# Kernel optimization log

Hardware: AMD Instinct MI355X
Metric: run time of the kernel (lower is better)

## Reference

```python
import jax, jax.numpy as jnp
import numpy as np

B, N, M, D = 4096, 39, 32, 32   # batch, fields, embed_dim, product_layer_dim
F = 1_000_000                   # features_dim (sparse vocab)
H = [400, 400, 400]             # hidden layer sizes
BN_EPS = 1e-3                   # keras BatchNormalization default epsilon


def setup_inputs() -> dict:
    key = jax.random.key(0)
    ks = jax.random.split(key, 32)
    inp = {
        "feature_index": jax.random.randint(ks[0], (B, N), 0, F),
        "feature_value": jax.random.normal(ks[1], (B, N), dtype=jnp.float32),
        # keras Embedding default 'uniform' initializer: U(-0.05, 0.05)
        "emb_table": jax.random.uniform(ks[2], (F, M), minval=-0.05, maxval=0.05, dtype=jnp.float32),
        "lin_w": jax.random.normal(ks[3], (D, N, M), dtype=jnp.float32) * 0.05,
        "quad_w": jax.random.normal(ks[4], (D, N), dtype=jnp.float32) * 0.1,
    }
    # MLP: input is concat(l_z, l_p) -> 2*D wide
    dims = [2 * D] + H
    k = 5
    for i in range(len(H)):
        fan_in, fan_out = dims[i], dims[i + 1]
        scale = (2.0 / (fan_in + fan_out)) ** 0.5
        inp[f"W{i}"] = jax.random.normal(ks[k], (fan_in, fan_out), dtype=jnp.float32) * scale; k += 1
        inp[f"b{i}"] = jnp.zeros((fan_out,), jnp.float32)
        inp[f"g{i}"] = jnp.ones((fan_out,), jnp.float32)    # BN gamma
        inp[f"be{i}"] = jnp.zeros((fan_out,), jnp.float32)  # BN beta
        inp[f"rm{i}"] = jnp.zeros((fan_out,), jnp.float32)  # BN moving mean
        inp[f"rv{i}"] = jnp.ones((fan_out,), jnp.float32)   # BN moving var
    inp["Wout"] = jax.random.normal(ks[k], (H[-1], 1), dtype=jnp.float32) * 0.05
    inp["bout"] = jnp.zeros((1,), jnp.float32)
    return inp


def _forward(feature_index, emb_table, lin_w, quad_w, layer_params, Wout, bout):
    e = emb_table[feature_index]                          # (B, N, M) embedding lookup
    l_z = jnp.einsum('bnm,dnm->bd', e, lin_w)             # linear signal
    theta = jnp.einsum('bnm,dn->bdnm', e, quad_w)         # IPNN quadratic signal
    l_p = jnp.einsum('bdnm,bdnm->bd', theta, theta)       # sum of squares over (n, m)
    x = jnp.concatenate([l_z, l_p], axis=1)               # (B, 2D)
    for (W, b, g, be, rm, rv) in layer_params:
        x = x @ W + b
        x = (x - rm) * jax.lax.rsqrt(rv + BN_EPS) * g + be  # BN (inference stats)
        x = jax.nn.relu(x)
    return jax.nn.sigmoid(x @ Wout + bout)                # (B, 1)


def reference(feature_index, feature_value, emb_table, lin_w, quad_w,
              W0, b0, g0, be0, rm0, rv0,
              W1, b1, g1, be1, rm1, rv1,
              W2, b2, g2, be2, rm2, rv2,
              Wout, bout):
    # feature_value is accepted by the original call() but never used; dropout disabled (eval).
    layer_params = [
        (W0, b0, g0, be0, rm0, rv0),
        (W1, b1, g1, be1, rm1, rv1),
        (W2, b2, g2, be2, rm2, rv2),
    ]
    return _forward(feature_index, emb_table, lin_w, quad_w, layer_params, Wout, bout)
```

## Files before the change

kernel.cpp:

```cpp
#include <hip/hip_runtime.h>
#include <hip/hip_bf16.h>
#include <math.h>

#define TB 4096
#define TN 39
#define TM 32
#define TD 32
#define TH 400
#define BN_EPS 1e-3f

#define KT0 2
#define KTH 13

typedef __attribute__((ext_vector_type(8))) short bf16x8;
typedef __attribute__((ext_vector_type(4))) float f32x4;

__device__ __forceinline__ ushort bf16_rn(float x) {
    __hip_bfloat16 h = __float2bfloat16(x);
    union { __hip_bfloat16 b; ushort u; } c; c.b = h; return c.u;
}
__device__ __forceinline__ void split2(float x, ushort& hi, ushort& lo) {
    unsigned xb = __float_as_uint(x);
    unsigned hb = xb & 0xFFFF0000u;
    hi = (ushort)(hb >> 16);
    lo = bf16_rn(x - __uint_as_float(hb));
}

__device__ __forceinline__ size_t panel_idx(int p, int k, int KT) {
    int lane_ = (p & 15) + 16 * ((k >> 2) & 3);
    int j_    = (k & 3) + 4 * ((k >> 4) & 1);
    return (((size_t)((p >> 4) * KT + (k >> 5)) * 64) + lane_) * 8 + j_;
}

__global__ __launch_bounds__(256) void fused_front_kernel(
    const int*   __restrict__ fidx,
    const float* __restrict__ emb,
    const float* __restrict__ lin_w,
    const float* __restrict__ quad_w,
    const float* __restrict__ W0, const float* __restrict__ W1, const float* __restrict__ W2,
    const float* __restrict__ b0_, const float* __restrict__ g0_, const float* __restrict__ be0_,
    const float* __restrict__ rm0_, const float* __restrict__ rv0_,
    const float* __restrict__ b1_, const float* __restrict__ g1_, const float* __restrict__ be1_,
    const float* __restrict__ rm1_, const float* __restrict__ rv1_,
    const float* __restrict__ b2_, const float* __restrict__ g2_, const float* __restrict__ be2_,
    const float* __restrict__ rm2_, const float* __restrict__ rv2_,
    ushort* __restrict__ A0h, ushort* __restrict__ A0l,
    ushort* __restrict__ B0h, ushort* __restrict__ B0l,
    ushort* __restrict__ B1h, ushort* __restrict__ B1l,
    ushort* __restrict__ B2h, ushort* __restrict__ B2l,
    float* __restrict__ AC)
{
    if (blockIdx.x >= TB / 4) {
        int tid = (blockIdx.x - TB / 4) * 256 + threadIdx.x;
        const int NW0 = 64 * 112, NW = 416 * 112;
        if (tid < NW0 + 2 * NW) {
            const float* W; ushort *Ph, *Pl; int k, n4, K, KT;
            if (tid < NW0) {
                W = W0; Ph = B0h; Pl = B0l; k = tid / 112; n4 = tid % 112; K = 64; KT = KT0;
            } else if (tid < NW0 + NW) {
                int u = tid - NW0;
                W = W1; Ph = B1h; Pl = B1l; k = u / 112; n4 = u % 112; K = TH; KT = KTH;
            } else {
                int u = tid - NW0 - NW;
                W = W2; Ph = B2h; Pl = B2l; k = u / 112; n4 = u % 112; K = TH; KT = KTH;
            }
            int n0 = n4 * 4;
            float4 w = make_float4(0.f, 0.f, 0.f, 0.f);
            if (k < K && n0 < TH)
                w = *(const float4*)&W[(size_t)k * TH + n0];
            float vals[4] = {w.x, w.y, w.z, w.w};
            #pragma unroll
            for (int i = 0; i < 4; ++i) {
                ushort hi, lo; split2(vals[i], hi, lo);
                size_t idx = panel_idx(n0 + i, k, KT);
                Ph[idx] = hi; Pl[idx] = lo;
            }
        } else if (tid < NW0 + 2 * NW + 3 * 448) {
            int u = tid - NW0 - 2 * NW;
            int layer = u / 448, h = u % 448;
            const float *gp, *bep, *rmp, *rvp, *bp;
            if (layer == 0)      { gp = g0_; bep = be0_; rmp = rm0_; rvp = rv0_; bp = b0_; }
            else if (layer == 1) { gp = g1_; bep = be1_; rmp = rm1_; rvp = rv1_; bp = b1_; }
            else                 { gp = g2_; bep = be2_; rmp = rm2_; rvp = rv2_; bp = b2_; }
            float aj = 0.f, cj = 0.f;
            if (h < TH) {
                aj = gp[h] * rsqrtf(rvp[h] + BN_EPS);
                cj = (bp[h] - rmp[h]) * aj + bep[h];
            }
            AC[layer * 896 + h] = aj;
            AC[layer * 896 + 448 + h] = cj;
        }
        return;
    }

    constexpr int R = 4;
    __shared__ float e_s[R][TN * TM];
    __shared__ int   idx_s[R][TN];
    __shared__ float s_s[R][TN];

    const int t  = threadIdx.x;
    const int b0 = blockIdx.x * R;

    if (t < R * TN) {
        int r = t / TN, n = t - r * TN;
        idx_s[r][n] = fidx[(b0 + r) * TN + n];
    }
    __syncthreads();

    for (int r = 0; r < R; ++r) {
        for (int k4 = t; k4 < TN * TM / 4; k4 += 256) {
            int n = k4 >> 3;
            long long base = (long long)idx_s[r][n] * TM + ((k4 & 7) << 2);
            *(float4*)&e_s[r][k4 * 4] = *(const float4*)&emb[base];
        }
    }
    __syncthreads();

    {
        const int d = t >> 3, j = t & 7;
        float acc[R] = {0.f, 0.f, 0.f, 0.f};
        const float* lw_base = lin_w + d * (TN * TM);
        #pragma unroll 4
        for (int i = 0; i < TN; ++i) {
            float4 lw = *(const float4*)&lw_base[i * 32 + j * 4];
            #pragma unroll
            for (int r = 0; r < R; ++r) {
                float4 e4 = *(const float4*)&e_s[r][i * 32 + j * 4];
                acc[r] = fmaf(lw.x, e4.x, acc[r]);
                acc[r] = fmaf(lw.y, e4.y, acc[r]);
                acc[r] = fmaf(lw.z, e4.z, acc[r]);
                acc[r] = fmaf(lw.w, e4.w, acc[r]);
            }
        }
        #pragma unroll
        for (int off = 1; off < 8; off <<= 1)
            #pragma unroll
            for (int r = 0; r < R; ++r)
                acc[r] += __shfl_xor(acc[r], off);
        if (j == 0) {
            #pragma unroll
            for (int r = 0; r < R; ++r) {
                ushort hi, lo; split2(acc[r], hi, lo);
                size_t idx = panel_idx(b0 + r, d, KT0);
                A0h[idx] = hi; A0l[idx] = lo;
            }
        }
    }

    {
        int r = t >> 6, lane = t & 63;
        if (lane < TN) {
            float s = 0.f;
            #pragma unroll
            for (int mm = 0; mm < TM; ++mm) {
                float v = e_s[r][lane * TM + ((lane + mm) & 31)];
                s = fmaf(v, v, s);
            }
            s_s[r][lane] = s;
        }
    }
    __syncthreads();

    if (t < R * TD) {
        int r = t >> 5, d = t & 31;
        float accv = 0.f;
        for (int n = 0; n < TN; ++n) {
            float q = quad_w[d * TN + n];
            accv = fmaf(s_s[r][n], q * q, accv);
        }
        ushort hi, lo; split2(accv, hi, lo);
        size_t idx = panel_idx(b0 + r, TD + d, KT0);
        A0h[idx] = hi; A0l[idx] = lo;
    }
}

template <int KT, int OUTMODE>
__global__ __launch_bounds__(256) void gemm_layer_v6(
    const ushort* __restrict__ Ah, const ushort* __restrict__ Al,
    const ushort* __restrict__ Bh, const ushort* __restrict__ Bl,
    const float* __restrict__ ACl,
    ushort* __restrict__ Nh, ushort* __restrict__ Nl,
    const float* __restrict__ Wout,
    float* __restrict__ P)
{
    const int lane = threadIdx.x & 63;
    const int wv   = threadIdx.x >> 6;
    const int msel = wv >> 1;
    const int nsel = wv & 1;

    const int orig = blockIdx.x;
    const int xcd  = orig & 7;
    const int slot = orig >> 3;
    const int bm   = (slot & 7) * 8 + xcd;
    const int bn   = slot >> 3;

    f32x4 acc[2][2];
    #pragma unroll
    for (int m = 0; m < 2; ++m)
        #pragma unroll
        for (int n = 0; n < 2; ++n)
            acc[m][n] = (f32x4){0.f, 0.f, 0.f, 0.f};

    const size_t lo8 = (size_t)lane * 8;
    const ushort* pAh = Ah + (size_t)(bm * 4 + msel * 2) * KT * 512 + lo8;
    const ushort* pAl = Al + (size_t)(bm * 4 + msel * 2) * KT * 512 + lo8;
    const ushort* pBh = Bh + (size_t)(bn * 4 + nsel * 2) * KT * 512 + lo8;
    const ushort* pBl = Bl + (size_t)(bn * 4 + nsel * 2) * KT * 512 + lo8;

    #pragma unroll 2
    for (int kt = 0; kt < KT; ++kt) {
        bf16x8 ah[2], al[2], bh[2], bl[2];
        #pragma unroll
        for (int m = 0; m < 2; ++m) {
            ah[m] = *(const bf16x8*)(pAh + (size_t)(m * KT + kt) * 512);
            al[m] = *(const bf16x8*)(pAl + (size_t)(m * KT + kt) * 512);
        }
        #pragma unroll
        for (int n = 0; n < 2; ++n) {
            bh[n] = *(const bf16x8*)(pBh + (size_t)(n * KT + kt) * 512);
            bl[n] = *(const bf16x8*)(pBl + (size_t)(n * KT + kt) * 512);
        }
        #pragma unroll
        for (int m = 0; m < 2; ++m)
            #pragma unroll
            for (int n = 0; n < 2; ++n) {
                acc[m][n] = __builtin_amdgcn_mfma_f32_16x16x32_bf16(ah[m], bh[n], acc[m][n], 0, 0, 0);
                acc[m][n] = __builtin_amdgcn_mfma_f32_16x16x32_bf16(ah[m], bl[n], acc[m][n], 0, 0, 0);
                acc[m][n] = __builtin_amdgcn_mfma_f32_16x16x32_bf16(al[m], bh[n], acc[m][n], 0, 0, 0);
            }
    }

    const int col = lane & 15, rq = (lane >> 4) << 2;

    if constexpr (OUTMODE == 0) {
        __shared__ float ysm[64][68];
        #pragma unroll
        for (int m = 0; m < 2; ++m)
            #pragma unroll
            for (int n = 0; n < 2; ++n) {
                int h = bn * 64 + (nsel * 2 + n) * 16 + col;
                float aj = ACl[h], cj = ACl[448 + h];
                #pragma unroll
                for (int r = 0; r < 4; ++r)
                    ysm[msel * 32 + m * 16 + rq + r][(nsel * 2 + n) * 16 + col] =
                        fmaxf(fmaf(acc[m][n][r], aj, cj), 0.f);
            }
        __syncthreads();

        const int ck = wv & 1;
        const int kt32 = bn * 2 + ck;
        if (kt32 < KTH) {
            #pragma unroll
            for (int mi = 0; mi < 2; ++mi) {
                int mtl = (wv >> 1) * 2 + mi;
                int row_l = mtl * 16 + (lane & 15);
                int kb = ck * 32 + rq;
                float4 v0 = *(const float4*)&ysm[row_l][kb];
                float4 v1 = *(const float4*)&ysm[row_l][kb + 16];
                ushort h_[8], l_[8];
                split2(v0.x, h_[0], l_[0]); split2(v0.y, h_[1], l_[1]);
                split2(v0.z, h_[2], l_[2]); split2(v0.w, h_[3], l_[3]);
                split2(v1.x, h_[4], l_[4]); split2(v1.y, h_[5], l_[5]);
                split2(v1.z, h_[6], l_[6]); split2(v1.w, h_[7], l_[7]);
                uint4 H, L;
                H.x = (uint)h_[0] | ((uint)h_[1] << 16);
                H.y = (uint)h_[2] | ((uint)h_[3] << 16);
                H.z = (uint)h_[4] | ((uint)h_[5] << 16);
                H.w = (uint)h_[6] | ((uint)h_[7] << 16);
                L.x = (uint)l_[0] | ((uint)l_[1] << 16);
                L.y = (uint)l_[2] | ((uint)l_[3] << 16);
                L.z = (uint)l_[4] | ((uint)l_[5] << 16);
                L.w = (uint)l_[6] | ((uint)l_[7] << 16);
                size_t base = (((size_t)(bm * 4 + mtl) * KTH + kt32) * 64 + lane) * 8;
                *(uint4*)(Nh + base) = H;
                *(uint4*)(Nl + base) = L;
            }
        }
    } else {
        float partial[2][4] = {{0.f,0.f,0.f,0.f},{0.f,0.f,0.f,0.f}};
        #pragma unroll
        for (int m = 0; m < 2; ++m)
            #pragma unroll
            for (int n = 0; n < 2; ++n) {
                int h = bn * 64 + (nsel * 2 + n) * 16 + col;
                float aj = ACl[h], cj = ACl[448 + h];
                float wv_ = (h < TH) ? Wout[h] : 0.f;
                #pragma unroll
                for (int r = 0; r < 4; ++r) {
                    float y = fmaxf(fmaf(acc[m][n][r], aj, cj), 0.f);
                    partial[m][r] = fmaf(y, wv_, partial[m][r]);
                }
            }
        #pragma unroll
        for (int off = 1; off < 16; off <<= 1)
            #pragma unroll
            for (int m = 0; m < 2; ++m)
                #pragma unroll
                for (int r = 0; r < 4; ++r)
                    partial[m][r] += __shfl_xor(partial[m][r], off);
        if (col == 0) {
            #pragma unroll
            for (int m = 0; m < 2; ++m)
                #pragma unroll
                for (int r = 0; r < 4; ++r)
                    P[(size_t)(bm * 64 + msel * 32 + m * 16 + rq + r) * 16
                      + bn * 2 + nsel] = partial[m][r];
        }
    }
}

__global__ __launch_bounds__(256) void fin_kernel(
    const float* __restrict__ P, const float* __restrict__ bout,
    float* __restrict__ out)
{
    int row = blockIdx.x * 256 + threadIdx.x;
    const float4* p = (const float4*)(P + (size_t)row * 16);
    float4 p0 = p[0], p1 = p[1], p2 = p[2], p3 = p[3];
    float s = bout[0]
            + p0.x + p0.y + p0.z + p0.w
            + p1.x + p1.y + p1.z + p1.w
            + p2.x + p2.y + p2.z + p2.w
            + p3.x + p3.y;
    out[row] = 1.f / (1.f + expf(-s));
}

extern "C" void kernel_launch(void* const* d_in, const int* in_sizes, int n_in,
                              void* d_out, int out_size, void* d_ws, size_t ws_size,
                              hipStream_t stream) {
    const int*   fidx   = (const int*)  d_in[0];
    const float* emb    = (const float*)d_in[2];
    const float* lin_w  = (const float*)d_in[3];
    const float* quad_w = (const float*)d_in[4];

    const float* W0  = (const float*)d_in[5];
    const float* b0  = (const float*)d_in[6];
    const float* g0  = (const float*)d_in[7];
    const float* be0 = (const float*)d_in[8];
    const float* rm0 = (const float*)d_in[9];
    const float* rv0 = (const float*)d_in[10];

    const float* W1  = (const float*)d_in[11];
    const float* b1  = (const float*)d_in[12];
    const float* g1  = (const float*)d_in[13];
    const float* be1 = (const float*)d_in[14];
    const float* rm1 = (const float*)d_in[15];
    const float* rv1 = (const float*)d_in[16];

    const float* W2  = (const float*)d_in[17];
    const float* b2  = (const float*)d_in[18];
    const float* g2  = (const float*)d_in[19];
    const float* be2 = (const float*)d_in[20];
    const float* rm2 = (const float*)d_in[21];
    const float* rv2 = (const float*)d_in[22];

    const float* Wout = (const float*)d_in[23];
    const float* bout = (const float*)d_in[24];

    const size_t SZ_A0 = (size_t)256 * KT0 * 512;
    const size_t SZ_A  = (size_t)256 * KTH * 512;
    const size_t SZ_B0 = (size_t)28  * KT0 * 512;
    const size_t SZ_B  = (size_t)28  * KTH * 512;

    ushort* p = (ushort*)d_ws;
    ushort *A0h = p; p += SZ_A0; ushort *A0l = p; p += SZ_A0;
    ushort *A1h = p; p += SZ_A;  ushort *A1l = p; p += SZ_A;
    ushort *A2h = p; p += SZ_A;  ushort *A2l = p; p += SZ_A;
    ushort *B0h = p; p += SZ_B0; ushort *B0l = p; p += SZ_B0;
    ushort *B1h = p; p += SZ_B;  ushort *B1l = p; p += SZ_B;
    ushort *B2h = p; p += SZ_B;  ushort *B2l = p; p += SZ_B;
    float*  AC  = (float*)p;
    float*  Pst = AC + 3 * 896;

    fused_front_kernel<<<TB / 4 + 398, 256, 0, stream>>>(
        fidx, emb, lin_w, quad_w, W0, W1, W2,
        b0, g0, be0, rm0, rv0,
        b1, g1, be1, rm1, rv1,
        b2, g2, be2, rm2, rv2,
        A0h, A0l, B0h, B0l, B1h, B1l, B2h, B2l, AC);

    gemm_layer_v6<KT0, 0><<<448, 256, 0, stream>>>(
        A0h, A0l, B0h, B0l, AC + 0, A1h, A1l, nullptr, nullptr);
    gemm_layer_v6<KTH, 0><<<448, 256, 0, stream>>>(
        A1h, A1l, B1h, B1l, AC + 896, A2h, A2l, nullptr, nullptr);
    gemm_layer_v6<KTH, 1><<<448, 256, 0, stream>>>(
        A2h, A2l, B2h, B2l, AC + 1792, nullptr, nullptr, Wout, Pst);

    fin_kernel<<<TB / 256, 256, 0, stream>>>(Pst, bout, (float*)d_out);
}
```

Baseline: 51.42 us.

## Process eight batch rows per front block with register-tiled linear projection

The front kernel now handles eight batch rows per block instead of four, which halves the number of embedding/projection blocks. The linear-signal loop is register-tiled: each thread computes 4 output dims × 2 rows, so each lin_w float4 load is reused across two rows and each embedding load across four dims. The aim is to cut global lin_w traffic per row and per-block overhead. In exchange, shared memory per block doubles, the per-row embedding stride gets padding, and fewer blocks may reduce the latency hiding available for the random embedding gathers.

```diff
diff --git a/kernel.cpp b/kernel.cpp
--- a/kernel.cpp
+++ b/kernel.cpp
@@ -11,6 +11,8 @@
 
 #define KT0 2
 #define KTH 13
+#define RGB 8
+#define ESP (TN * TM + 8)
 
 typedef __attribute__((ext_vector_type(8))) short bf16x8;
 typedef __attribute__((ext_vector_type(4))) float f32x4;
@@ -50,8 +52,8 @@
     ushort* __restrict__ B2h, ushort* __restrict__ B2l,
     float* __restrict__ AC)
 {
-    if (blockIdx.x >= TB / 4) {
-        int tid = (blockIdx.x - TB / 4) * 256 + threadIdx.x;
+    if (blockIdx.x >= TB / RGB) {
+        int tid = (blockIdx.x - TB / RGB) * 256 + threadIdx.x;
         const int NW0 = 64 * 112, NW = 416 * 112;
         if (tid < NW0 + 2 * NW) {
             const float* W; ushort *Ph, *Pl; int k, n4, K, KT;
@@ -93,21 +95,20 @@
         return;
     }
 
-    constexpr int R = 4;
-    __shared__ float e_s[R][TN * TM];
-    __shared__ int   idx_s[R][TN];
-    __shared__ float s_s[R][TN];
+    __shared__ float e_s[RGB][ESP];
+    __shared__ int   idx_s[RGB][TN];
+    __shared__ float s_s[RGB][TN];
 
     const int t  = threadIdx.x;
-    const int b0 = blockIdx.x * R;
-
-    if (t < R * TN) {
-        int r = t / TN, n = t - r * TN;
+    const int b0 = blockIdx.x * RGB;
+
+    for (int u = t; u < RGB * TN; u += 256) {
+        int r = u / TN, n = u - r * TN;
         idx_s[r][n] = fidx[(b0 + r) * TN + n];
     }
     __syncthreads();
 
-    for (int r = 0; r < R; ++r) {
+    for (int r = 0; r < RGB; ++r) {
         for (int k4 = t; k4 < TN * TM / 4; k4 += 256) {
             int n = k4 >> 3;
             long long base = (long long)idx_s[r][n] * TM + ((k4 & 7) << 2);
@@ -117,51 +118,66 @@
     __syncthreads();
 
     {
-        const int d = t >> 3, j = t & 7;
-        float acc[R] = {0.f, 0.f, 0.f, 0.f};
-        const float* lw_base = lin_w + d * (TN * TM);
+        const int dg = t >> 5, rs = (t >> 3) & 3, j = t & 7;
+        const int mo = j * 4;
+        float acc[4][2] = {};
+        const float* lw0 = lin_w + (size_t)(dg * 4) * (TN * TM) + mo;
+        const float* er0 = &e_s[rs * 2][0];
+        const float* er1 = &e_s[rs * 2 + 1][0];
         #pragma unroll 4
         for (int i = 0; i < TN; ++i) {
-            float4 lw = *(const float4*)&lw_base[i * 32 + j * 4];
-            #pragma unroll
-            for (int r = 0; r < R; ++r) {
-                float4 e4 = *(const float4*)&e_s[r][i * 32 + j * 4];
-                acc[r] = fmaf(lw.x, e4.x, acc[r]);
-                acc[r] = fmaf(lw.y, e4.y, acc[r]);
-                acc[r] = fmaf(lw.z, e4.z, acc[r]);
-                acc[r] = fmaf(lw.w, e4.w, acc[r]);
+            float4 lw[4];
+            #pragma unroll
+            for (int di = 0; di < 4; ++di)
+                lw[di] = *(const float4*)(lw0 + (size_t)di * (TN * TM) + i * 32);
+            float4 e0 = *(const float4*)(er0 + i * 32 + mo);
+            float4 e1 = *(const float4*)(er1 + i * 32 + mo);
+            #pragma unroll
+            for (int di = 0; di < 4; ++di) {
+                acc[di][0] = fmaf(lw[di].x, e0.x, acc[di][0]);
+                acc[di][0] = fmaf(lw[di].y, e0.y, acc[di][0]);
+                acc[di][0] = fmaf(lw[di].z, e0.z, acc[di][0]);
+                acc[di][0] = fmaf(lw[di].w, e0.w, acc[di][0]);
+                acc[di][1] = fmaf(lw[di].x, e1.x, acc[di][1]);
+                acc[di][1] = fmaf(lw[di].y, e1.y, acc[di][1]);
+                acc[di][1] = fmaf(lw[di].z, e1.z, acc[di][1]);
+                acc[di][1] = fmaf(lw[di].w, e1.w, acc[di][1]);
             }
         }
         #pragma unroll
         for (int off = 1; off < 8; off <<= 1)
             #pragma unroll
-            for (int r = 0; r < R; ++r)
-                acc[r] += __shfl_xor(acc[r], off);
+            for (int di = 0; di < 4; ++di)
+                #pragma unroll
+                for (int rr = 0; rr < 2; ++rr)
+                    acc[di][rr] += __shfl_xor(acc[di][rr], off);
         if (j == 0) {
             #pragma unroll
-            for (int r = 0; r < R; ++r) {
-                ushort hi, lo; split2(acc[r], hi, lo);
-                size_t idx = panel_idx(b0 + r, d, KT0);
-                A0h[idx] = hi; A0l[idx] = lo;
-            }
+            for (int di = 0; di < 4; ++di)
+                #pragma unroll
+                for (int rr = 0; rr < 2; ++rr) {
+                    ushort hi, lo; split2(acc[di][rr], hi, lo);
+                    size_t idx = panel_idx(b0 + rs * 2 + rr, dg * 4 + di, KT0);
+                    A0h[idx] = hi; A0l[idx] = lo;
+                }
         }
     }
 
     {
-        int r = t >> 6, lane = t & 63;
-        if (lane < TN) {
+        int r = t >> 5, sub = t & 31;
+        for (int n = sub; n < TN; n += 32) {
             float s = 0.f;
             #pragma unroll
             for (int mm = 0; mm < TM; ++mm) {
-                float v = e_s[r][lane * TM + ((lane + mm) & 31)];
+                float v = e_s[r][n * TM + ((n + mm) & 31)];
                 s = fmaf(v, v, s);
             }
-            s_s[r][lane] = s;
+            s_s[r][n] = s;
         }
     }
     __syncthreads();
 
-    if (t < R * TD) {
+    {
         int r = t >> 5, d = t & 31;
         float accv = 0.f;
         for (int n = 0; n < TN; ++n) {
@@ -371,7 +387,7 @@
     float*  AC  = (float*)p;
     float*  Pst = AC + 3 * 896;
 
-    fused_front_kernel<<<TB / 4 + 398, 256, 0, stream>>>(
+    fused_front_kernel<<<TB / RGB + 398, 256, 0, stream>>>(
         fidx, emb, lin_w, quad_w, W0, W1, W2,
         b0, g0, be0, rm0, rv0,
         b1, g1, be1, rm1, rv1,
```

Result: slower. 56.30 us (+9.5%).

## Double-buffer GEMM operand tiles in LDS via global_load_lds prefetch

Applied to the files above, without the earlier changes.

The layer GEMM kernels now stage A/B hi/lo panel tiles into a two-slot shared-memory buffer with direct global-to-LDS loads, prefetching the next k-tile while MFMAs run on the current one. Previously every wave loaded its operands straight from global memory, and tiles shared between waves were fetched more than once. The epilogue reuses the staging buffer for the activation scratch, so shared-memory use stays about the same. The cost is a barrier on every k-iteration, which matters with only 2 or 13 k-steps, and a correctness risk: no explicit vmcnt wait is visible before the barrier, so the loads into LDS may not be guaranteed complete when they are read.

```diff
diff --git a/kernel.cpp b/kernel.cpp
--- a/kernel.cpp
+++ b/kernel.cpp
@@ -24,6 +24,13 @@
     unsigned hb = xb & 0xFFFF0000u;
     hi = (ushort)(hb >> 16);
     lo = bf16_rn(x - __uint_as_float(hb));
+}
+
+__device__ __forceinline__ void gload_lds16(const ushort* g, ushort* l) {
+    __builtin_amdgcn_global_load_lds(
+        (const __attribute__((address_space(1))) void*)g,
+        (__attribute__((address_space(3))) void*)l,
+        16, 0, 0);
 }
 
 __device__ __forceinline__ size_t panel_idx(int p, int k, int KT) {
@@ -175,7 +182,7 @@
 }
 
 template <int KT, int OUTMODE>
-__global__ __launch_bounds__(256) void gemm_layer_v6(
+__global__ __launch_bounds__(256) void gemm_layer_v7(
     const ushort* __restrict__ Ah, const ushort* __restrict__ Al,
     const ushort* __restrict__ Bh, const ushort* __restrict__ Bl,
     const float* __restrict__ ACl,
@@ -183,6 +190,8 @@
     const float* __restrict__ Wout,
     float* __restrict__ P)
 {
+    __shared__ ushort stage[2][16 * 512];
+
     const int lane = threadIdx.x & 63;
     const int wv   = threadIdx.x >> 6;
     const int msel = wv >> 1;
@@ -194,6 +203,20 @@
     const int bm   = (slot & 7) * 8 + xcd;
     const int bn   = slot >> 3;
 
+    const ushort* csrc[4];
+    int coff[4];
+    #pragma unroll
+    for (int i = 0; i < 4; ++i) {
+        int c = wv * 4 + i;
+        bool isA = c < 8;
+        int tl  = isA ? (c >> 1) : ((c - 8) >> 1);
+        bool lo = c & 1;
+        const ushort* base = isA ? (lo ? Al : Ah) : (lo ? Bl : Bh);
+        int tileIdx = isA ? (bm * 4 + tl) : (bn * 4 + tl);
+        csrc[i] = base + (size_t)tileIdx * KT * 512 + (size_t)lane * 8;
+        coff[i] = c * 512;
+    }
+
     f32x4 acc[2][2];
     #pragma unroll
     for (int m = 0; m < 2; ++m)
@@ -201,24 +224,32 @@
         for (int n = 0; n < 2; ++n)
             acc[m][n] = (f32x4){0.f, 0.f, 0.f, 0.f};
 
-    const size_t lo8 = (size_t)lane * 8;
-    const ushort* pAh = Ah + (size_t)(bm * 4 + msel * 2) * KT * 512 + lo8;
-    const ushort* pAl = Al + (size_t)(bm * 4 + msel * 2) * KT * 512 + lo8;
-    const ushort* pBh = Bh + (size_t)(bn * 4 + nsel * 2) * KT * 512 + lo8;
-    const ushort* pBl = Bl + (size_t)(bn * 4 + nsel * 2) * KT * 512 + lo8;
-
-    #pragma unroll 2
+    #pragma unroll
+    for (int i = 0; i < 4; ++i)
+        gload_lds16(csrc[i], &stage[0][coff[i]]);
+    __syncthreads();
+
     for (int kt = 0; kt < KT; ++kt) {
+        const int cur = kt & 1;
+        if (kt + 1 < KT) {
+            #pragma unroll
+            for (int i = 0; i < 4; ++i)
+                gload_lds16(csrc[i] + (size_t)(kt + 1) * 512,
+                            &stage[cur ^ 1][coff[i]]);
+        }
+        const ushort* L = &stage[cur][0];
         bf16x8 ah[2], al[2], bh[2], bl[2];
         #pragma unroll
         for (int m = 0; m < 2; ++m) {
-            ah[m] = *(const bf16x8*)(pAh + (size_t)(m * KT + kt) * 512);
-            al[m] = *(const bf16x8*)(pAl + (size_t)(m * KT + kt) * 512);
+            int mt = msel * 2 + m;
+            ah[m] = *(const bf16x8*)&L[(mt * 2 + 0) * 512 + lane * 8];
+            al[m] = *(const bf16x8*)&L[(mt * 2 + 1) * 512 + lane * 8];
         }
         #pragma unroll
         for (int n = 0; n < 2; ++n) {
-            bh[n] = *(const bf16x8*)(pBh + (size_t)(n * KT + kt) * 512);
-            bl[n] = *(const bf16x8*)(pBl + (size_t)(n * KT + kt) * 512);
+            int nt = nsel * 2 + n;
+            bh[n] = *(const bf16x8*)&L[(8 + nt * 2 + 0) * 512 + lane * 8];
+            bl[n] = *(const bf16x8*)&L[(8 + nt * 2 + 1) * 512 + lane * 8];
         }
         #pragma unroll
         for (int m = 0; m < 2; ++m)
@@ -228,12 +259,13 @@
                 acc[m][n] = __builtin_amdgcn_mfma_f32_16x16x32_bf16(ah[m], bl[n], acc[m][n], 0, 0, 0);
                 acc[m][n] = __builtin_amdgcn_mfma_f32_16x16x32_bf16(al[m], bh[n], acc[m][n], 0, 0, 0);
             }
+        __syncthreads();
     }
 
     const int col = lane & 15, rq = (lane >> 4) << 2;
 
     if constexpr (OUTMODE == 0) {
-        __shared__ float ysm[64][68];
+        float (*ysm)[68] = (float (*)[68])(void*)&stage[0][0];
         #pragma unroll
         for (int m = 0; m < 2; ++m)
             #pragma unroll
@@ -262,18 +294,18 @@
                 split2(v0.z, h_[2], l_[2]); split2(v0.w, h_[3], l_[3]);
                 split2(v1.x, h_[4], l_[4]); split2(v1.y, h_[5], l_[5]);
                 split2(v1.z, h_[6], l_[6]); split2(v1.w, h_[7], l_[7]);
-                uint4 H, L;
+                uint4 H, L2;
                 H.x = (uint)h_[0] | ((uint)h_[1] << 16);
                 H.y = (uint)h_[2] | ((uint)h_[3] << 16);
                 H.z = (uint)h_[4] | ((uint)h_[5] << 16);
                 H.w = (uint)h_[6] | ((uint)h_[7] << 16);
-                L.x = (uint)l_[0] | ((uint)l_[1] << 16);
-                L.y = (uint)l_[2] | ((uint)l_[3] << 16);
-                L.z = (uint)l_[4] | ((uint)l_[5] << 16);
-                L.w = (uint)l_[6] | ((uint)l_[7] << 16);
+                L2.x = (uint)l_[0] | ((uint)l_[1] << 16);
+                L2.y = (uint)l_[2] | ((uint)l_[3] << 16);
+                L2.z = (uint)l_[4] | ((uint)l_[5] << 16);
+                L2.w = (uint)l_[6] | ((uint)l_[7] << 16);
                 size_t base = (((size_t)(bm * 4 + mtl) * KTH + kt32) * 64 + lane) * 8;
                 *(uint4*)(Nh + base) = H;
-                *(uint4*)(Nl + base) = L;
+                *(uint4*)(Nl + base) = L2;
             }
         }
     } else {
@@ -378,11 +410,11 @@
         b2, g2, be2, rm2, rv2,
         A0h, A0l, B0h, B0l, B1h, B1l, B2h, B2l, AC);
 
-    gemm_layer_v6<KT0, 0><<<448, 256, 0, stream>>>(
+    gemm_layer_v7<KT0, 0><<<448, 256, 0, stream>>>(
         A0h, A0l, B0h, B0l, AC + 0, A1h, A1l, nullptr, nullptr);
-    gemm_layer_v6<KTH, 0><<<448, 256, 0, stream>>>(
+    gemm_layer_v7<KTH, 0><<<448, 256, 0, stream>>>(
         A1h, A1l, B1h, B1l, AC + 896, A2h, A2l, nullptr, nullptr);
-    gemm_layer_v6<KTH, 1><<<448, 256, 0, stream>>>(
+    gemm_layer_v7<KTH, 1><<<448, 256, 0, stream>>>(
         A2h, A2l, B2h, B2l, AC + 1792, nullptr, nullptr, Wout, Pst);
 
     fin_kernel<<<TB / 256, 256, 0, stream>>>(Pst, bout, (float*)d_out);
```

New measurement: 47.27 us (median of 2 runs). -8.1%, faster.
